# Performance work log

Measured on AMD Instinct MI355X. Metric: run time of the kernel, lower is better.

Reference implementation:

```python
import jax, jax.numpy as jnp
import numpy as np

N_NODES = 50000
N_EDGES = 640000
IN_FEATS = 128
HID = 128


def setup_inputs() -> dict:
    key = jax.random.key(0)
    ks = jax.random.split(key, 8)
    x = jax.random.normal(ks[0], (N_NODES, IN_FEATS), dtype=jnp.float32)
    src = jax.random.randint(ks[1], (N_EDGES,), 0, N_NODES, dtype=jnp.int32)
    dst = jax.random.randint(ks[2], (N_EDGES,), 0, N_NODES, dtype=jnp.int32)
    s1 = 1.0 / np.sqrt(IN_FEATS)
    s2 = 1.0 / np.sqrt(HID)
    W1 = jax.random.normal(ks[3], (IN_FEATS, HID), dtype=jnp.float32) * s1
    b1 = jnp.zeros((HID,), dtype=jnp.float32)
    W2 = jax.random.normal(ks[4], (HID, HID), dtype=jnp.float32) * s2
    b2 = jnp.zeros((HID,), dtype=jnp.float32)
    Wr = jax.random.normal(ks[5], (HID, 2), dtype=jnp.float32) * s2
    br = jnp.zeros((2,), dtype=jnp.float32)
    return {"x": x, "src": src, "dst": dst, "W1": W1, "b1": b1,
            "W2": W2, "b2": b2, "Wr": Wr, "br": br}


def _degree_norm(idx, n):
    # D^{-1/2}, with 0 for zero-degree nodes (DGL sets inf -> 0)
    deg = jax.ops.segment_sum(jnp.ones(idx.shape[0], jnp.float32), idx, num_segments=n)
    return jnp.where(deg > 0, jax.lax.rsqrt(jnp.maximum(deg, 1.0)), 0.0)


def _graph_conv(h, W, b, src, dst, norm_out, norm_in, n):
    # DGL GraphConv, norm='both': out = D_in^{-1/2} A D_out^{-1/2} (h W) + b
    hW = (h * norm_out[:, None]) @ W          # [N, hid]
    agg = jax.ops.segment_sum(hW[src], dst, num_segments=n)  # gather+scatter over edges
    return agg * norm_in[:, None] + b


def reference(x, src, dst, W1, b1, W2, b2, Wr, br):
    n = x.shape[0]
    norm_out = _degree_norm(src, n)  # source-side out-degree norm
    norm_in = _degree_norm(dst, n)   # dest-side in-degree norm
    h = jax.nn.relu(_graph_conv(x, W1, b1, src, dst, norm_out, norm_in, n))
    h = jax.nn.relu(_graph_conv(h, W2, b2, src, dst, norm_out, norm_in, n))
    hg = jnp.mean(h, axis=0, keepdims=True)  # [1, hid]
    return hg @ Wr + br                      # [1, 2]
```

## Files before the change

kernel.cpp:

```cpp
#include <hip/hip_runtime.h>
#include <hip/hip_bf16.h>

#define FEAT 128
#define RBITS 12
#define RSIZE 4096
#define NCHUNK 64

typedef __attribute__((ext_vector_type(8))) short short8;
typedef __attribute__((ext_vector_type(4))) short short4v;
typedef __attribute__((ext_vector_type(4))) float f32x4;

__device__ __forceinline__ ushort f2bf(float f) {
    union { float f; unsigned u; } v; v.f = f;
    unsigned u = v.u;
    unsigned r = 0x7fffu + ((u >> 16) & 1u);
    return (ushort)((u + r) >> 16);
}
__device__ __forceinline__ float bf2f(short s) {
    union { unsigned u; float f; } v;
    v.u = ((unsigned)(ushort)s) << 16;
    return v.f;
}

__global__ __launch_bounds__(256)
void hist_kernel(const int* __restrict__ src, const int* __restrict__ dst,
                 unsigned* __restrict__ partial, int E, int CS)
{
    __shared__ unsigned hist[RSIZE];
    const int c = blockIdx.x, p = blockIdx.y, job = blockIdx.z;
    const int* __restrict__ idx = job ? dst : src;
    for (int r = threadIdx.x; r < RSIZE; r += 256) hist[r] = 0;
    __syncthreads();
    const int e0 = c * CS, e1 = min(E, e0 + CS);
    for (int e = e0 + threadIdx.x; e < e1; e += 256) {
        int v = idx[e];
        if ((v >> RBITS) == p) atomicAdd(&hist[v & (RSIZE - 1)], 1u);
    }
    __syncthreads();
    unsigned* out = partial +
        (((size_t)job * gridDim.y + p) * NCHUNK + c) * RSIZE;
    for (int r = threadIdx.x; r < RSIZE; r += 256) out[r] = hist[r];
}

__global__ __launch_bounds__(256)
void merge_kernel(unsigned* __restrict__ partialOut, unsigned* __restrict__ partialIn,
                  int* __restrict__ cntIn, float* __restrict__ normOut,
                  float* __restrict__ normIn, int N)
{
    int n = blockIdx.x * 256 + threadIdx.x;
    if (n >= N) return;
    const int p = n >> RBITS, r = n & (RSIZE - 1);
    const size_t base = (size_t)p * NCHUNK * RSIZE + r;
    unsigned so = 0;
#pragma unroll 8
    for (int c = 0; c < NCHUNK; ++c) so += partialOut[base + (size_t)c * RSIZE];
    unsigned off = 0;
#pragma unroll 8
    for (int c = 0; c < NCHUNK; ++c) {
        size_t i = base + (size_t)c * RSIZE;
        unsigned t = partialIn[i];
        partialIn[i] = off;
        off += t;
    }
    cntIn[n]   = (int)off;
    normIn[n]  = off ? rsqrtf((float)off) : 0.0f;
    normOut[n] = so  ? rsqrtf((float)so)  : 0.0f;
}

__global__ __launch_bounds__(256)
void scan1_kernel(const int* __restrict__ cnt, int* __restrict__ blockSums, int N)
{
    __shared__ int sh[256];
    int i = blockIdx.x * 256 + threadIdx.x;
    sh[threadIdx.x] = (i < N) ? cnt[i] : 0;
    __syncthreads();
    for (int off = 128; off > 0; off >>= 1) {
        if (threadIdx.x < off) sh[threadIdx.x] += sh[threadIdx.x + off];
        __syncthreads();
    }
    if (threadIdx.x == 0) blockSums[blockIdx.x] = sh[0];
}

__global__ __launch_bounds__(256)
void rowstart_kernel(const int* __restrict__ cntIn, const int* __restrict__ blockSums,
                     int* __restrict__ rowStart, int N, int NB, int E)
{
    __shared__ int bs[256];
    __shared__ int bse[256];
    __shared__ int sh[256];
    const int t = threadIdx.x;
    int bv = (t < NB) ? blockSums[t] : 0;
    bs[t] = bv;
    __syncthreads();
    for (int off = 1; off < 256; off <<= 1) {
        int u = (t >= off) ? bs[t - off] : 0;
        __syncthreads();
        bs[t] += u;
        __syncthreads();
    }
    bse[t] = bs[t] - bv;
    __syncthreads();

    const int i = blockIdx.x * 256 + t;
    int v = (i < N) ? cntIn[i] : 0;
    sh[t] = v;
    __syncthreads();
    for (int off = 1; off < 256; off <<= 1) {
        int u = (t >= off) ? sh[t - off] : 0;
        __syncthreads();
        sh[t] += u;
        __syncthreads();
    }
    if (i < N) rowStart[i] = bse[blockIdx.x] + sh[t] - v;
    if (blockIdx.x == 0 && t == 0) rowStart[N] = E;
}

__global__ __launch_bounds__(256)
void fill_kernel(const int* __restrict__ src, const int* __restrict__ dst,
                 const int* __restrict__ rowStart, const unsigned* __restrict__ chunkOff,
                 int* __restrict__ csrSrc, int N, int E, int CS)
{
    __shared__ unsigned cursor[RSIZE];
    const int c = blockIdx.x, p = blockIdx.y;
    const unsigned* co = chunkOff + ((size_t)p * NCHUNK + c) * RSIZE;
    for (int r = threadIdx.x; r < RSIZE; r += 256) {
        int n = (p << RBITS) + r;
        cursor[r] = (n < N) ? (unsigned)rowStart[n] + co[r] : 0u;
    }
    __syncthreads();
    const int e0 = c * CS, e1 = min(E, e0 + CS);
    for (int e = e0 + threadIdx.x; e < e1; e += 256) {
        int d = dst[e];
        if ((d >> RBITS) == p) {
            unsigned pos = atomicAdd(&cursor[d & (RSIZE - 1)], 1u);
            csrSrc[pos] = src[e];
        }
    }
}

template<bool F32IN>
__global__ __launch_bounds__(256)
void gemm_mfma_kernel(const void* __restrict__ Ain, const float* __restrict__ W,
                      const float* __restrict__ scale, ushort* __restrict__ C,
                      int M, int nStrips)
{
    __shared__ ushort WT[128 * 132];
    __shared__ ushort As[64 * 132];
    __shared__ float  sScale[64];

    const int tid  = threadIdx.x;
    const int wv   = tid >> 6;
    const int lane = tid & 63;
    const int rowHalf = wv >> 1;
    const int colHalf = wv & 1;
    const int l15  = lane & 15;
    const int quad = lane >> 4;

    for (int it = 0; it < 16; ++it) {
        int fid = tid + (it << 8);
        int k   = fid >> 5;
        int c4  = (fid & 31) << 2;
        float4 w = *(const float4*)(W + (size_t)k * FEAT + c4);
        WT[(c4 + 0) * 132 + k] = f2bf(w.x);
        WT[(c4 + 1) * 132 + k] = f2bf(w.y);
        WT[(c4 + 2) * 132 + k] = f2bf(w.z);
        WT[(c4 + 3) * 132 + k] = f2bf(w.w);
    }
    __syncthreads();

    short8 bfrag[4][4];
#pragma unroll
    for (int ct = 0; ct < 4; ++ct) {
        int col = colHalf * 64 + ct * 16 + l15;
#pragma unroll
        for (int kst = 0; kst < 4; ++kst) {
            int k = kst * 32 + quad * 8;
            short4v lo = *(const short4v*)&WT[col * 132 + k];
            short4v hi = *(const short4v*)&WT[col * 132 + k + 4];
            bfrag[ct][kst] = __builtin_shufflevector(lo, hi, 0, 1, 2, 3, 4, 5, 6, 7);
        }
    }

    for (int s = blockIdx.x; s < nStrips; s += gridDim.x) {
        const int row0 = s << 6;
        __syncthreads();

#pragma unroll
        for (int it = 0; it < 4; ++it) {
            int fid = tid + (it << 8);
            int r   = fid >> 4;
            int seg = (fid & 15) << 3;
            int grow = row0 + r;
            short4v lo = {0, 0, 0, 0}, hi = {0, 0, 0, 0};
            if (grow < M) {
                if (F32IN) {
                    const float* pa = (const float*)Ain + (size_t)grow * FEAT + seg;
                    float4 u0 = *(const float4*)(pa);
                    float4 u1 = *(const float4*)(pa + 4);
                    lo[0] = (short)f2bf(u0.x); lo[1] = (short)f2bf(u0.y);
                    lo[2] = (short)f2bf(u0.z); lo[3] = (short)f2bf(u0.w);
                    hi[0] = (short)f2bf(u1.x); hi[1] = (short)f2bf(u1.y);
                    hi[2] = (short)f2bf(u1.z); hi[3] = (short)f2bf(u1.w);
                } else {
                    const ushort* pa = (const ushort*)Ain + (size_t)grow * FEAT + seg;
                    lo = *(const short4v*)(pa);
                    hi = *(const short4v*)(pa + 4);
                }
            }
            *(short4v*)&As[r * 132 + seg]     = lo;
            *(short4v*)&As[r * 132 + seg + 4] = hi;
        }
        if (tid < 64) {
            int grow = row0 + tid;
            sScale[tid] = (grow < M) ? scale[grow] : 0.0f;
        }
        __syncthreads();

        f32x4 acc[2][4] = {};
#pragma unroll
        for (int kst = 0; kst < 4; ++kst) {
            int k = kst * 32 + quad * 8;
            short8 af[2];
#pragma unroll
            for (int rt = 0; rt < 2; ++rt) {
                int row = rowHalf * 32 + rt * 16 + l15;
                short4v lo = *(const short4v*)&As[row * 132 + k];
                short4v hi = *(const short4v*)&As[row * 132 + k + 4];
                af[rt] = __builtin_shufflevector(lo, hi, 0, 1, 2, 3, 4, 5, 6, 7);
            }
#pragma unroll
            for (int rt = 0; rt < 2; ++rt)
#pragma unroll
                for (int ct = 0; ct < 4; ++ct)
                    acc[rt][ct] = __builtin_amdgcn_mfma_f32_16x16x32_bf16(
                        af[rt], bfrag[ct][kst], acc[rt][ct], 0, 0, 0);
        }

#pragma unroll
        for (int rt = 0; rt < 2; ++rt) {
            int rbase = rowHalf * 32 + rt * 16 + quad * 4;
#pragma unroll
            for (int reg = 0; reg < 4; ++reg) {
                int rl = rbase + reg;
                int grow = row0 + rl;
                if (grow < M) {
                    float sc = sScale[rl];
#pragma unroll
                    for (int ct = 0; ct < 4; ++ct) {
                        int col = colHalf * 64 + ct * 16 + l15;
                        C[(size_t)grow * FEAT + col] = f2bf(acc[rt][ct][reg] * sc);
                    }
                }
            }
        }
    }
}

__global__ __launch_bounds__(256)
void gather_kernel(const ushort* __restrict__ t, const int* __restrict__ rowStart,
                   const int* __restrict__ csrSrc, const float* __restrict__ normIn,
                   const float* __restrict__ bias, ushort* __restrict__ out, int N)
{
    const int hw   = threadIdx.x >> 5;
    const int lane = threadIdx.x & 31;
    const int node = blockIdx.x * 8 + hw;
    if (node >= N) return;
    const int s = rowStart[node];
    const int e = rowStart[node + 1];
    float a0 = 0.f, a1 = 0.f, a2 = 0.f, a3 = 0.f;
    for (int base = s; base < e; base += 32) {
        const int m = min(32, e - base);
        int idx = (base + lane < e) ? csrSrc[base + lane] : 0;
        int j = 0;
        for (; j + 4 <= m; j += 4) {
            int s0 = __shfl(idx, j,     32);
            int s1 = __shfl(idx, j + 1, 32);
            int s2 = __shfl(idx, j + 2, 32);
            int s3 = __shfl(idx, j + 3, 32);
            short4v v0 = *(const short4v*)(t + (size_t)s0 * FEAT + lane * 4);
            short4v v1 = *(const short4v*)(t + (size_t)s1 * FEAT + lane * 4);
            short4v v2 = *(const short4v*)(t + (size_t)s2 * FEAT + lane * 4);
            short4v v3 = *(const short4v*)(t + (size_t)s3 * FEAT + lane * 4);
            a0 += bf2f(v0[0]) + bf2f(v1[0]) + bf2f(v2[0]) + bf2f(v3[0]);
            a1 += bf2f(v0[1]) + bf2f(v1[1]) + bf2f(v2[1]) + bf2f(v3[1]);
            a2 += bf2f(v0[2]) + bf2f(v1[2]) + bf2f(v2[2]) + bf2f(v3[2]);
            a3 += bf2f(v0[3]) + bf2f(v1[3]) + bf2f(v2[3]) + bf2f(v3[3]);
        }
        for (; j < m; ++j) {
            int srcn = __shfl(idx, j, 32);
            short4v v = *(const short4v*)(t + (size_t)srcn * FEAT + lane * 4);
            a0 += bf2f(v[0]); a1 += bf2f(v[1]); a2 += bf2f(v[2]); a3 += bf2f(v[3]);
        }
    }
    float ni = normIn[node];
    float4 b = *(const float4*)(bias + lane * 4);
    short4v o;
    o[0] = (short)f2bf(fmaxf(fmaf(a0, ni, b.x), 0.0f));
    o[1] = (short)f2bf(fmaxf(fmaf(a1, ni, b.y), 0.0f));
    o[2] = (short)f2bf(fmaxf(fmaf(a2, ni, b.z), 0.0f));
    o[3] = (short)f2bf(fmaxf(fmaf(a3, ni, b.w), 0.0f));
    *(short4v*)(out + (size_t)node * FEAT + lane * 4) = o;
}

__global__ __launch_bounds__(256)
void colreduce_kernel(const ushort* __restrict__ h2, float* __restrict__ colsum, int N)
{
    const int c  = threadIdx.x & 127;
    const int rg = threadIdx.x >> 7;
    const int r0 = blockIdx.x * 256;
    const int rEnd = min(r0 + 256, N);
    float acc = 0.0f;
    for (int r = r0 + rg; r < rEnd; r += 2)
        acc += bf2f(h2[(size_t)r * FEAT + c]);
    __shared__ float sh[256];
    sh[threadIdx.x] = acc;
    __syncthreads();
    if (rg == 0) unsafeAtomicAdd(&colsum[c], sh[c] + sh[128 + c]);
}

__global__ __launch_bounds__(128)
void final_kernel(const float* __restrict__ colsum, const float* __restrict__ Wr,
                  const float* __restrict__ br, float* __restrict__ out, float invN)
{
    __shared__ float s0[128], s1[128];
    int j = threadIdx.x;
    float hg = colsum[j] * invN;
    s0[j] = hg * Wr[2 * j + 0];
    s1[j] = hg * Wr[2 * j + 1];
    __syncthreads();
    for (int off = 64; off > 0; off >>= 1) {
        if (j < off) { s0[j] += s0[j + off]; s1[j] += s1[j + off]; }
        __syncthreads();
    }
    if (j == 0) {
        out[0] = s0[0] + br[0];
        out[1] = s1[0] + br[1];
    }
}

extern "C" void kernel_launch(void* const* d_in, const int* in_sizes, int n_in,
                              void* d_out, int out_size, void* d_ws, size_t ws_size,
                              hipStream_t stream)
{
    const float* x   = (const float*)d_in[0];
    const int*   src = (const int*)d_in[1];
    const int*   dst = (const int*)d_in[2];
    const float* W1  = (const float*)d_in[3];
    const float* b1  = (const float*)d_in[4];
    const float* W2  = (const float*)d_in[5];
    const float* b2  = (const float*)d_in[6];
    const float* Wr  = (const float*)d_in[7];
    const float* br  = (const float*)d_in[8];
    float* out = (float*)d_out;

    const int N = in_sizes[0] / FEAT;
    const int E = in_sizes[1];
    const int NP = ((N + 255) / 256) * 256;
    const int NB = (N + 255) / 256;
    const int P  = (N + RSIZE - 1) / RSIZE;
    const int CS = (E + NCHUNK - 1) / NCHUNK;

    char* p = (char*)d_ws;
    unsigned* partial   = (unsigned*)p;  p += (size_t)2 * P * NCHUNK * RSIZE * 4;
    float*  colsum    = (float*)p;       p += 256 * 4;
    int*    blockSums = (int*)p;         p += 256 * 4;
    int*    cntIn     = (int*)p;         p += (size_t)NP * 4;
    float*  normOut   = (float*)p;       p += (size_t)NP * 4;
    float*  normIn    = (float*)p;       p += (size_t)NP * 4;
    int*    rowStart  = (int*)p;         p += (size_t)(NP + 64) * 4;
    int*    csrSrc    = (int*)p;         p += (size_t)E * 4;
    ushort* bufT      = (ushort*)p;      p += (size_t)N * FEAT * 2;
    ushort* bufH      = (ushort*)p;      p += (size_t)N * FEAT * 2;

    unsigned* partialOut = partial;
    unsigned* partialIn  = partial + (size_t)P * NCHUNK * RSIZE;

    hipMemsetAsync(colsum, 0, 256 * 4, stream);

    hist_kernel<<<dim3(NCHUNK, P, 2), 256, 0, stream>>>(src, dst, partial, E, CS);
    merge_kernel<<<NB, 256, 0, stream>>>(partialOut, partialIn, cntIn, normOut, normIn, N);
    scan1_kernel<<<NB, 256, 0, stream>>>(cntIn, blockSums, N);
    rowstart_kernel<<<NB, 256, 0, stream>>>(cntIn, blockSums, rowStart, N, NB, E);
    fill_kernel<<<dim3(NCHUNK, P), 256, 0, stream>>>(src, dst, rowStart, partialIn, csrSrc, N, E, CS);

    const int nStrips = (N + 63) / 64;
    const int gathBlocks = (N + 7) / 8;

    gemm_mfma_kernel<true><<<256, 256, 0, stream>>>((const void*)x, W1, normOut, bufT, N, nStrips);
    gather_kernel<<<gathBlocks, 256, 0, stream>>>(bufT, rowStart, csrSrc, normIn, b1, bufH, N);

    gemm_mfma_kernel<false><<<256, 256, 0, stream>>>((const void*)bufH, W2, normOut, bufT, N, nStrips);
    gather_kernel<<<gathBlocks, 256, 0, stream>>>(bufT, rowStart, csrSrc, normIn, b2, bufH, N);

    colreduce_kernel<<<NB, 256, 0, stream>>>(bufH, colsum, N);
    final_kernel<<<1, 128, 0, stream>>>(colsum, Wr, br, out, 1.0f / (float)N);
}
```

Baseline: 260.0 us.

## Pack per-chunk degree histograms into bytes and fuse preprocessing kernels

Per-chunk degree counts are now stored as 8-bit counters packed four per word, with src and dst counted in a single pass. The partition size doubles, and this is meant to cut partial-histogram traffic, LDS use and the number of blocks. The block-sum scan is fused into the merge kernel, and zeroing colsum moves into rowstart, which removes a kernel launch and a memset. The GEMM drops its persistent-strip loop and uses one block per 64-row strip, so B fragments are reloaded from LDS each k-step instead of being held in registers. Byte counters overflow if a node gets more than 255 edges within one chunk, which random inputs avoid but skewed graphs would not.

```diff
diff --git a/kernel.cpp b/kernel.cpp
--- a/kernel.cpp
+++ b/kernel.cpp
@@ -2,8 +2,8 @@
 #include <hip/hip_bf16.h>
 
 #define FEAT 128
-#define RBITS 12
-#define RSIZE 4096
+#define RBITS 13
+#define RSIZE 8192
 #define NCHUNK 64
 
 typedef __attribute__((ext_vector_type(8))) short short8;
@@ -24,58 +24,64 @@
 
 __global__ __launch_bounds__(256)
 void hist_kernel(const int* __restrict__ src, const int* __restrict__ dst,
-                 unsigned* __restrict__ partial, int E, int CS)
-{
-    __shared__ unsigned hist[RSIZE];
-    const int c = blockIdx.x, p = blockIdx.y, job = blockIdx.z;
-    const int* __restrict__ idx = job ? dst : src;
-    for (int r = threadIdx.x; r < RSIZE; r += 256) hist[r] = 0;
+                 unsigned* __restrict__ partialSrc, unsigned* __restrict__ partialDst,
+                 int E, int CS)
+{
+    __shared__ unsigned hs[RSIZE / 4];
+    __shared__ unsigned hd[RSIZE / 4];
+    const int c = blockIdx.x, p = blockIdx.y;
+    for (int r = threadIdx.x; r < RSIZE / 4; r += 256) { hs[r] = 0; hd[r] = 0; }
     __syncthreads();
     const int e0 = c * CS, e1 = min(E, e0 + CS);
     for (int e = e0 + threadIdx.x; e < e1; e += 256) {
-        int v = idx[e];
-        if ((v >> RBITS) == p) atomicAdd(&hist[v & (RSIZE - 1)], 1u);
-    }
-    __syncthreads();
-    unsigned* out = partial +
-        (((size_t)job * gridDim.y + p) * NCHUNK + c) * RSIZE;
-    for (int r = threadIdx.x; r < RSIZE; r += 256) out[r] = hist[r];
-}
-
-__global__ __launch_bounds__(256)
-void merge_kernel(unsigned* __restrict__ partialOut, unsigned* __restrict__ partialIn,
+        int s = src[e];
+        if ((s >> RBITS) == p) {
+            int r = s & (RSIZE - 1);
+            atomicAdd(&hs[r >> 2], 1u << ((r & 3) * 8));
+        }
+        int d = dst[e];
+        if ((d >> RBITS) == p) {
+            int r = d & (RSIZE - 1);
+            atomicAdd(&hd[r >> 2], 1u << ((r & 3) * 8));
+        }
+    }
+    __syncthreads();
+    const size_t base = ((size_t)p * NCHUNK + c) * (RSIZE / 4);
+    for (int r = threadIdx.x; r < RSIZE / 4; r += 256) {
+        partialSrc[base + r] = hs[r];
+        partialDst[base + r] = hd[r];
+    }
+}
+
+__global__ __launch_bounds__(256)
+void merge_kernel(const unsigned char* __restrict__ ps8, unsigned char* __restrict__ pd8,
                   int* __restrict__ cntIn, float* __restrict__ normOut,
-                  float* __restrict__ normIn, int N)
-{
-    int n = blockIdx.x * 256 + threadIdx.x;
-    if (n >= N) return;
-    const int p = n >> RBITS, r = n & (RSIZE - 1);
-    const size_t base = (size_t)p * NCHUNK * RSIZE + r;
-    unsigned so = 0;
+                  float* __restrict__ normIn, int* __restrict__ blockSums, int N)
+{
+    const int n = blockIdx.x * 256 + threadIdx.x;
+    unsigned off = 0;
+    if (n < N) {
+        const int p = n >> RBITS, r = n & (RSIZE - 1);
+        const size_t base = (size_t)p * NCHUNK * RSIZE + r;
+        unsigned so = 0;
 #pragma unroll 8
-    for (int c = 0; c < NCHUNK; ++c) so += partialOut[base + (size_t)c * RSIZE];
-    unsigned off = 0;
+        for (int c = 0; c < NCHUNK; ++c) so += ps8[base + (size_t)c * RSIZE];
 #pragma unroll 8
-    for (int c = 0; c < NCHUNK; ++c) {
-        size_t i = base + (size_t)c * RSIZE;
-        unsigned t = partialIn[i];
-        partialIn[i] = off;
-        off += t;
-    }
-    cntIn[n]   = (int)off;
-    normIn[n]  = off ? rsqrtf((float)off) : 0.0f;
-    normOut[n] = so  ? rsqrtf((float)so)  : 0.0f;
-}
-
-__global__ __launch_bounds__(256)
-void scan1_kernel(const int* __restrict__ cnt, int* __restrict__ blockSums, int N)
-{
+        for (int c = 0; c < NCHUNK; ++c) {
+            size_t i = base + (size_t)c * RSIZE;
+            unsigned t = pd8[i];
+            pd8[i] = (unsigned char)off;
+            off += t;
+        }
+        cntIn[n]   = (int)off;
+        normIn[n]  = off ? rsqrtf((float)off) : 0.0f;
+        normOut[n] = so  ? rsqrtf((float)so)  : 0.0f;
+    }
     __shared__ int sh[256];
-    int i = blockIdx.x * 256 + threadIdx.x;
-    sh[threadIdx.x] = (i < N) ? cnt[i] : 0;
-    __syncthreads();
-    for (int off = 128; off > 0; off >>= 1) {
-        if (threadIdx.x < off) sh[threadIdx.x] += sh[threadIdx.x + off];
+    sh[threadIdx.x] = (int)off;
+    __syncthreads();
+    for (int o = 128; o > 0; o >>= 1) {
+        if (threadIdx.x < o) sh[threadIdx.x] += sh[threadIdx.x + o];
         __syncthreads();
     }
     if (threadIdx.x == 0) blockSums[blockIdx.x] = sh[0];
@@ -83,7 +89,8 @@
 
 __global__ __launch_bounds__(256)
 void rowstart_kernel(const int* __restrict__ cntIn, const int* __restrict__ blockSums,
-                     int* __restrict__ rowStart, int N, int NB, int E)
+                     int* __restrict__ rowStart, float* __restrict__ colsum,
+                     int N, int NB, int E)
 {
     __shared__ int bs[256];
     __shared__ int bse[256];
@@ -112,20 +119,23 @@
         __syncthreads();
     }
     if (i < N) rowStart[i] = bse[blockIdx.x] + sh[t] - v;
-    if (blockIdx.x == 0 && t == 0) rowStart[N] = E;
+    if (blockIdx.x == 0) {
+        if (t == 0) rowStart[N] = E;
+        colsum[t] = 0.0f;
+    }
 }
 
 __global__ __launch_bounds__(256)
 void fill_kernel(const int* __restrict__ src, const int* __restrict__ dst,
-                 const int* __restrict__ rowStart, const unsigned* __restrict__ chunkOff,
+                 const int* __restrict__ rowStart, const unsigned char* __restrict__ chunkOff8,
                  int* __restrict__ csrSrc, int N, int E, int CS)
 {
     __shared__ unsigned cursor[RSIZE];
     const int c = blockIdx.x, p = blockIdx.y;
-    const unsigned* co = chunkOff + ((size_t)p * NCHUNK + c) * RSIZE;
+    const unsigned char* co = chunkOff8 + ((size_t)p * NCHUNK + c) * RSIZE;
     for (int r = threadIdx.x; r < RSIZE; r += 256) {
         int n = (p << RBITS) + r;
-        cursor[r] = (n < N) ? (unsigned)rowStart[n] + co[r] : 0u;
+        cursor[r] = (n < N) ? (unsigned)rowStart[n] + (unsigned)co[r] : 0u;
     }
     __syncthreads();
     const int e0 = c * CS, e1 = min(E, e0 + CS);
@@ -141,8 +151,7 @@
 template<bool F32IN>
 __global__ __launch_bounds__(256)
 void gemm_mfma_kernel(const void* __restrict__ Ain, const float* __restrict__ W,
-                      const float* __restrict__ scale, ushort* __restrict__ C,
-                      int M, int nStrips)
+                      const float* __restrict__ scale, ushort* __restrict__ C, int M)
 {
     __shared__ ushort WT[128 * 132];
     __shared__ ushort As[64 * 132];
@@ -155,6 +164,7 @@
     const int colHalf = wv & 1;
     const int l15  = lane & 15;
     const int quad = lane >> 4;
+    const int row0 = blockIdx.x << 6;
 
     for (int it = 0; it < 16; ++it) {
         int fid = tid + (it << 8);
@@ -166,90 +176,78 @@
         WT[(c4 + 2) * 132 + k] = f2bf(w.z);
         WT[(c4 + 3) * 132 + k] = f2bf(w.w);
     }
-    __syncthreads();
-
-    short8 bfrag[4][4];
-#pragma unroll
-    for (int ct = 0; ct < 4; ++ct) {
-        int col = colHalf * 64 + ct * 16 + l15;
-#pragma unroll
-        for (int kst = 0; kst < 4; ++kst) {
-            int k = kst * 32 + quad * 8;
+#pragma unroll
+    for (int it = 0; it < 4; ++it) {
+        int fid = tid + (it << 8);
+        int r   = fid >> 4;
+        int seg = (fid & 15) << 3;
+        int grow = row0 + r;
+        short4v lo = {0, 0, 0, 0}, hi = {0, 0, 0, 0};
+        if (grow < M) {
+            if (F32IN) {
+                const float* pa = (const float*)Ain + (size_t)grow * FEAT + seg;
+                float4 u0 = *(const float4*)(pa);
+                float4 u1 = *(const float4*)(pa + 4);
+                lo[0] = (short)f2bf(u0.x); lo[1] = (short)f2bf(u0.y);
+                lo[2] = (short)f2bf(u0.z); lo[3] = (short)f2bf(u0.w);
+                hi[0] = (short)f2bf(u1.x); hi[1] = (short)f2bf(u1.y);
+                hi[2] = (short)f2bf(u1.z); hi[3] = (short)f2bf(u1.w);
+            } else {
+                const ushort* pa = (const ushort*)Ain + (size_t)grow * FEAT + seg;
+                lo = *(const short4v*)(pa);
+                hi = *(const short4v*)(pa + 4);
+            }
+        }
+        *(short4v*)&As[r * 132 + seg]     = lo;
+        *(short4v*)&As[r * 132 + seg + 4] = hi;
+    }
+    if (tid < 64) {
+        int grow = row0 + tid;
+        sScale[tid] = (grow < M) ? scale[grow] : 0.0f;
+    }
+    __syncthreads();
+
+    f32x4 acc[2][4] = {};
+#pragma unroll
+    for (int kst = 0; kst < 4; ++kst) {
+        int k = kst * 32 + quad * 8;
+        short8 af[2];
+#pragma unroll
+        for (int rt = 0; rt < 2; ++rt) {
+            int row = rowHalf * 32 + rt * 16 + l15;
+            short4v lo = *(const short4v*)&As[row * 132 + k];
+            short4v hi = *(const short4v*)&As[row * 132 + k + 4];
+            af[rt] = __builtin_shufflevector(lo, hi, 0, 1, 2, 3, 4, 5, 6, 7);
+        }
+        short8 bf[4];
+#pragma unroll
+        for (int ct = 0; ct < 4; ++ct) {
+            int col = colHalf * 64 + ct * 16 + l15;
             short4v lo = *(const short4v*)&WT[col * 132 + k];
             short4v hi = *(const short4v*)&WT[col * 132 + k + 4];
-            bfrag[ct][kst] = __builtin_shufflevector(lo, hi, 0, 1, 2, 3, 4, 5, 6, 7);
-        }
-    }
-
-    for (int s = blockIdx.x; s < nStrips; s += gridDim.x) {
-        const int row0 = s << 6;
-        __syncthreads();
-
-#pragma unroll
-        for (int it = 0; it < 4; ++it) {
-            int fid = tid + (it << 8);
-            int r   = fid >> 4;
-            int seg = (fid & 15) << 3;
-            int grow = row0 + r;
-            short4v lo = {0, 0, 0, 0}, hi = {0, 0, 0, 0};
+            bf[ct] = __builtin_shufflevector(lo, hi, 0, 1, 2, 3, 4, 5, 6, 7);
+        }
+#pragma unroll
+        for (int rt = 0; rt < 2; ++rt)
+#pragma unroll
+            for (int ct = 0; ct < 4; ++ct)
+                acc[rt][ct] = __builtin_amdgcn_mfma_f32_16x16x32_bf16(
+                    af[rt], bf[ct], acc[rt][ct], 0, 0, 0);
+    }
+
+#pragma unroll
+    for (int rt = 0; rt < 2; ++rt) {
+        int rbase = rowHalf * 32 + rt * 16 + quad * 4;
+#pragma unroll
+        for (int reg = 0; reg < 4; ++reg) {
+            int rl = rbase + reg;
+            int grow = row0 + rl;
             if (grow < M) {
-                if (F32IN) {
-                    const float* pa = (const float*)Ain + (size_t)grow * FEAT + seg;
-                    float4 u0 = *(const float4*)(pa);
-                    float4 u1 = *(const float4*)(pa + 4);
-                    lo[0] = (short)f2bf(u0.x); lo[1] = (short)f2bf(u0.y);
-                    lo[2] = (short)f2bf(u0.z); lo[3] = (short)f2bf(u0.w);
-                    hi[0] = (short)f2bf(u1.x); hi[1] = (short)f2bf(u1.y);
-                    hi[2] = (short)f2bf(u1.z); hi[3] = (short)f2bf(u1.w);
-                } else {
-                    const ushort* pa = (const ushort*)Ain + (size_t)grow * FEAT + seg;
-                    lo = *(const short4v*)(pa);
-                    hi = *(const short4v*)(pa + 4);
-                }
-            }
-            *(short4v*)&As[r * 132 + seg]     = lo;
-            *(short4v*)&As[r * 132 + seg + 4] = hi;
-        }
-        if (tid < 64) {
-            int grow = row0 + tid;
-            sScale[tid] = (grow < M) ? scale[grow] : 0.0f;
-        }
-        __syncthreads();
-
-        f32x4 acc[2][4] = {};
-#pragma unroll
-        for (int kst = 0; kst < 4; ++kst) {
-            int k = kst * 32 + quad * 8;
-            short8 af[2];
-#pragma unroll
-            for (int rt = 0; rt < 2; ++rt) {
-                int row = rowHalf * 32 + rt * 16 + l15;
-                short4v lo = *(const short4v*)&As[row * 132 + k];
-                short4v hi = *(const short4v*)&As[row * 132 + k + 4];
-                af[rt] = __builtin_shufflevector(lo, hi, 0, 1, 2, 3, 4, 5, 6, 7);
-            }
-#pragma unroll
-            for (int rt = 0; rt < 2; ++rt)
-#pragma unroll
-                for (int ct = 0; ct < 4; ++ct)
-                    acc[rt][ct] = __builtin_amdgcn_mfma_f32_16x16x32_bf16(
-                        af[rt], bfrag[ct][kst], acc[rt][ct], 0, 0, 0);
-        }
-
-#pragma unroll
-        for (int rt = 0; rt < 2; ++rt) {
-            int rbase = rowHalf * 32 + rt * 16 + quad * 4;
-#pragma unroll
-            for (int reg = 0; reg < 4; ++reg) {
-                int rl = rbase + reg;
-                int grow = row0 + rl;
-                if (grow < M) {
-                    float sc = sScale[rl];
-#pragma unroll
-                    for (int ct = 0; ct < 4; ++ct) {
-                        int col = colHalf * 64 + ct * 16 + l15;
-                        C[(size_t)grow * FEAT + col] = f2bf(acc[rt][ct][reg] * sc);
-                    }
+                float sc = sScale[rl];
+#pragma unroll
+                for (int ct = 0; ct < 4; ++ct) {
+                    int col = colHalf * 64 + ct * 16 + l15;
+                    C[(size_t)grow * FEAT + col] = f2bf(acc[rt][ct][reg] * sc);
                 }
             }
         }
@@ -361,35 +359,34 @@
     const int CS = (E + NCHUNK - 1) / NCHUNK;
 
     char* p = (char*)d_ws;
-    unsigned* partial   = (unsigned*)p;  p += (size_t)2 * P * NCHUNK * RSIZE * 4;
-    float*  colsum    = (float*)p;       p += 256 * 4;
-    int*    blockSums = (int*)p;         p += 256 * 4;
-    int*    cntIn     = (int*)p;         p += (size_t)NP * 4;
-    float*  normOut   = (float*)p;       p += (size_t)NP * 4;
-    float*  normIn    = (float*)p;       p += (size_t)NP * 4;
-    int*    rowStart  = (int*)p;         p += (size_t)(NP + 64) * 4;
-    int*    csrSrc    = (int*)p;         p += (size_t)E * 4;
-    ushort* bufT      = (ushort*)p;      p += (size_t)N * FEAT * 2;
-    ushort* bufH      = (ushort*)p;      p += (size_t)N * FEAT * 2;
-
-    unsigned* partialOut = partial;
-    unsigned* partialIn  = partial + (size_t)P * NCHUNK * RSIZE;
-
-    hipMemsetAsync(colsum, 0, 256 * 4, stream);
-
-    hist_kernel<<<dim3(NCHUNK, P, 2), 256, 0, stream>>>(src, dst, partial, E, CS);
-    merge_kernel<<<NB, 256, 0, stream>>>(partialOut, partialIn, cntIn, normOut, normIn, N);
-    scan1_kernel<<<NB, 256, 0, stream>>>(cntIn, blockSums, N);
-    rowstart_kernel<<<NB, 256, 0, stream>>>(cntIn, blockSums, rowStart, N, NB, E);
-    fill_kernel<<<dim3(NCHUNK, P), 256, 0, stream>>>(src, dst, rowStart, partialIn, csrSrc, N, E, CS);
+    unsigned* partialSrc = (unsigned*)p;  p += (size_t)P * NCHUNK * (RSIZE / 4) * 4;
+    unsigned* partialDst = (unsigned*)p;  p += (size_t)P * NCHUNK * (RSIZE / 4) * 4;
+    float*  colsum    = (float*)p;        p += 256 * 4;
+    int*    blockSums = (int*)p;          p += 256 * 4;
+    int*    cntIn     = (int*)p;          p += (size_t)NP * 4;
+    float*  normOut   = (float*)p;        p += (size_t)NP * 4;
+    float*  normIn    = (float*)p;        p += (size_t)NP * 4;
+    int*    rowStart  = (int*)p;          p += (size_t)(NP + 64) * 4;
+    int*    csrSrc    = (int*)p;          p += (size_t)E * 4;
+    ushort* bufT      = (ushort*)p;       p += (size_t)N * FEAT * 2;
+    ushort* bufH      = (ushort*)p;       p += (size_t)N * FEAT * 2;
+
+    hist_kernel<<<dim3(NCHUNK, P), 256, 0, stream>>>(src, dst, partialSrc, partialDst, E, CS);
+    merge_kernel<<<NB, 256, 0, stream>>>((const unsigned char*)partialSrc,
+                                         (unsigned char*)partialDst,
+                                         cntIn, normOut, normIn, blockSums, N);
+    rowstart_kernel<<<NB, 256, 0, stream>>>(cntIn, blockSums, rowStart, colsum, N, NB, E);
+    fill_kernel<<<dim3(NCHUNK, P), 256, 0, stream>>>(src, dst, rowStart,
+                                                     (const unsigned char*)partialDst,
+                                                     csrSrc, N, E, CS);
 
     const int nStrips = (N + 63) / 64;
     const int gathBlocks = (N + 7) / 8;
 
-    gemm_mfma_kernel<true><<<256, 256, 0, stream>>>((const void*)x, W1, normOut, bufT, N, nStrips);
+    gemm_mfma_kernel<true><<<nStrips, 256, 0, stream>>>((const void*)x, W1, normOut, bufT, N);
     gather_kernel<<<gathBlocks, 256, 0, stream>>>(bufT, rowStart, csrSrc, normIn, b1, bufH, N);
 
-    gemm_mfma_kernel<false><<<256, 256, 0, stream>>>((const void*)bufH, W2, normOut, bufT, N, nStrips);
+    gemm_mfma_kernel<false><<<nStrips, 256, 0, stream>>>((const void*)bufH, W2, normOut, bufT, N);
     gather_kernel<<<gathBlocks, 256, 0, stream>>>(bufT, rowStart, csrSrc, normIn, b2, bufH, N);
 
     colreduce_kernel<<<NB, 256, 0, stream>>>(bufH, colsum, N);
```

New measurement: 260.8 us. About the same (+0.3%).
